# Kernel optimization log

Hardware: AMD Instinct MI355X
Metric: run time of the kernel (lower is better)

Reference implementation:

```python
import jax, jax.numpy as jnp
import numpy as np

N_USERS, N_ITEMS, D, B = 16384, 4096, 64, 2048
NAN_FRAC = 0.7
EPS = 1e-8


def setup_inputs() -> dict:
    key = jax.random.key(0)
    k1, k2, k3, k4, k5 = jax.random.split(key, 5)
    ratings = jax.random.uniform(k1, (N_USERS, N_ITEMS), jnp.float32, 1.0, 5.0)
    miss = jax.random.uniform(k2, (N_USERS, N_ITEMS)) < NAN_FRAC
    rating_matrix = jnp.where(miss, jnp.nan, ratings)
    user_embeddings = jax.random.normal(k3, (N_USERS, D), jnp.float32)
    user_indices = jax.random.randint(k4, (B,), 0, N_USERS)
    item_indices = jax.random.randint(k5, (B,), 0, N_ITEMS)
    return {
        "rating_matrix": rating_matrix,
        "user_embeddings": user_embeddings,
        "user_indices": user_indices,
        "item_indices": item_indices,
    }


def reference(rating_matrix, user_embeddings, user_indices, item_indices):
    n_users = rating_matrix.shape[0]

    # per-user average over non-NaN ratings (0.0 if user has no ratings)
    valid_r = ~jnp.isnan(rating_matrix)                      # [N, I]
    r0 = jnp.where(valid_r, rating_matrix, 0.0)
    cnt = valid_r.sum(axis=1)
    avg_ratings = jnp.where(cnt > 0, r0.sum(axis=1) / jnp.maximum(cnt, 1), 0.0)  # [N]

    u = user_embeddings[user_indices]                        # [B, d]
    # cosine similarity of each query user vs all users
    dots = jnp.einsum('bd,nd->bn', u, user_embeddings)       # [B, N]
    mag_u = jnp.linalg.norm(u, axis=1, keepdims=True)        # [B, 1]
    mag_v = jnp.linalg.norm(user_embeddings, axis=1)[None]   # [1, N]
    sim = dots / (mag_u * mag_v + EPS)                       # [B, N]

    # ratings of all users on each query item
    ratings_col = rating_matrix[:, item_indices].T           # [B, N]
    mask = ~jnp.isnan(ratings_col)                           # valid neighbor ratings
    mask = mask & (jnp.arange(n_users)[None, :] != user_indices[:, None])  # exclude self

    diff = jnp.where(mask, ratings_col - avg_ratings[None, :], 0.0)
    sim_m = jnp.where(mask, sim, 0.0)
    num = (diff * sim_m).sum(axis=1)                         # [B]
    den = jnp.abs(sim_m).sum(axis=1)                         # [B]
    den_safe = jnp.where(den == 0, 1.0, den)

    avg_u = avg_ratings[user_indices]
    return jnp.where(den == 0, avg_u, avg_u + num / den_safe)
```

## Files before the change

kernel.cpp:

```cpp
#include <hip/hip_runtime.h>
#include <math.h>

#define NU   16384
#define NI   4096
#define DDIM 64
#define BB   2048
#define GSTR8 2056

typedef unsigned short u16;
typedef unsigned char  u8;
typedef __attribute__((ext_vector_type(8))) short short8;
typedef __attribute__((ext_vector_type(4))) float f32x4;

static __device__ __forceinline__ u16 f2bf(float f) {
    union { float f; unsigned int u; } v; v.f = f;
    unsigned int u = v.u + 0x7FFFu + ((v.u >> 16) & 1u);
    return (u16)(u >> 16);
}

static __device__ __forceinline__ u8 enc_r(float r) {
    return (r == r) ? (u8)(__float2int_rn((r - 1.0f) * 50.0f) + 1) : (u8)0;
}

__global__ __launch_bounds__(256) void k_qprep(
    const float* __restrict__ E, const int* __restrict__ uidx,
    u16* __restrict__ Ubf, int2* __restrict__ qinfo)
{
    const int lane = threadIdx.x & 63;
    const int b = blockIdx.x * 4 + (threadIdx.x >> 6);
    const int ub = uidx[b];
    const float e = E[(size_t)ub * DDIM + lane];
    float ss = e * e;
#pragma unroll
    for (int o = 32; o > 0; o >>= 1) ss += __shfl_xor(ss, o);
    Ubf[b * DDIM + lane] = f2bf(e);
    if (lane == 0) qinfo[b] = make_int2(ub, __float_as_int(rsqrtf(ss)));
}

__global__ __launch_bounds__(256) void k_fused(
    const float* __restrict__ R, const float* __restrict__ E,
    const int* __restrict__ iidx, const u16* __restrict__ Ubf,
    const int2* __restrict__ qinfo, float2* __restrict__ partials,
    float* __restrict__ avgAll)
{
    __shared__ u16 s_ii[BB];
    __shared__ u8  rowq[2][NI];
    __shared__ u8  g[16][GSTR8];
    __shared__ float sAvg[16], sInv[16];
    __shared__ float redS[2][4], redC[2][4];

    const int tid  = threadIdx.x;
    const int lane = tid & 63;
    const int wid  = tid >> 6;
    const int n0   = blockIdx.x * 16;

    for (int t = tid; t < BB; t += 256) s_ii[t] = (u16)iidx[t];

#pragma unroll
    for (int rs = 0; rs < 4; ++rs) {
        const int n = n0 + wid * 4 + rs;
        const float e = E[(size_t)n * DDIM + lane];
        float ss = e * e;
#pragma unroll
        for (int o = 32; o > 0; o >>= 1) ss += __shfl_xor(ss, o);
        if (lane == 0) sInv[wid * 4 + rs] = rsqrtf(ss);
    }

    float4 vv[4];
    {
        const float4* R4 = (const float4*)(R + (size_t)n0 * NI);
#pragma unroll
        for (int j = 0; j < 4; ++j) vv[j] = R4[tid + j * 256];
    }

#pragma unroll 1
    for (int rr = 0; rr < 16; ++rr) {
        const int p = rr & 1;

        float4 vn[4];
        {
            const int np = n0 + ((rr < 15) ? rr + 1 : 15);
            const float4* Rn = (const float4*)(R + (size_t)np * NI);
#pragma unroll
            for (int j = 0; j < 4; ++j) vn[j] = Rn[tid + j * 256];
        }

        float sum = 0.f, cnt = 0.f;
#pragma unroll
        for (int j = 0; j < 4; ++j) {
            const float4 v = vv[j];
            if (v.x == v.x) { sum += v.x; cnt += 1.f; }
            if (v.y == v.y) { sum += v.y; cnt += 1.f; }
            if (v.z == v.z) { sum += v.z; cnt += 1.f; }
            if (v.w == v.w) { sum += v.w; cnt += 1.f; }
            uchar4 q;
            q.x = enc_r(v.x); q.y = enc_r(v.y); q.z = enc_r(v.z); q.w = enc_r(v.w);
            *(uchar4*)&rowq[p][(tid + j * 256) * 4] = q;
        }
#pragma unroll
        for (int o = 32; o > 0; o >>= 1) {
            sum += __shfl_xor(sum, o);
            cnt += __shfl_xor(cnt, o);
        }
        if (lane == 0) { redS[p][wid] = sum; redC[p][wid] = cnt; }

        __syncthreads();

        if (tid == 0) {
            const float S = redS[p][0] + redS[p][1] + redS[p][2] + redS[p][3];
            const float C = redC[p][0] + redC[p][1] + redC[p][2] + redC[p][3];
            const float a = (C > 0.f) ? (S / C) : 0.f;
            sAvg[rr] = a;
            avgAll[n0 + rr] = a;
        }
#pragma unroll
        for (int t = 0; t < 2; ++t) {
            const int b4 = (tid + t * 256) * 4;
            const ushort4 ii = *(const ushort4*)&s_ii[b4];
            uchar4 q;
            q.x = rowq[p][ii.x]; q.y = rowq[p][ii.y];
            q.z = rowq[p][ii.z]; q.w = rowq[p][ii.w];
            *(uchar4*)&g[rr][b4] = q;
        }
#pragma unroll
        for (int j = 0; j < 4; ++j) vv[j] = vn[j];
    }
    __syncthreads();

    const int lo = lane & 15;
    const int hi = lane >> 4;

    short8 a[2];
#pragma unroll
    for (int kg = 0; kg < 2; ++kg) {
        const float* ep = E + (size_t)(n0 + lo) * DDIM + kg * 32 + hi * 8;
        const float4 e0 = *(const float4*)(ep);
        const float4 e1 = *(const float4*)(ep + 4);
        union { short8 v; u16 u[8]; } t;
        t.u[0] = f2bf(e0.x); t.u[1] = f2bf(e0.y); t.u[2] = f2bf(e0.z); t.u[3] = f2bf(e0.w);
        t.u[4] = f2bf(e1.x); t.u[5] = f2bf(e1.y); t.u[6] = f2bf(e1.z); t.u[7] = f2bf(e1.w);
        a[kg] = t.v;
    }
    float avr[4], ivr[4];
#pragma unroll
    for (int r = 0; r < 4; ++r) { avr[r] = sAvg[hi * 4 + r]; ivr[r] = sInv[hi * 4 + r]; }

    float2* pout = partials + (size_t)blockIdx.x * BB;

#pragma unroll 1
    for (int j = 0; j < 32; ++j) {
        const int b0 = (j * 4 + wid) * 16;
        const int2 q = qinfo[b0 + lo];
        const float inv_mu = __int_as_float(q.y);

        const short8 bf0 = *(const short8*)(Ubf + (size_t)(b0 + lo) * DDIM + hi * 8);
        const short8 bf1 = *(const short8*)(Ubf + (size_t)(b0 + lo) * DDIM + 32 + hi * 8);

        f32x4 c = {0.f, 0.f, 0.f, 0.f};
        c = __builtin_amdgcn_mfma_f32_16x16x32_bf16(a[0], bf0, c, 0, 0, 0);
        c = __builtin_amdgcn_mfma_f32_16x16x32_bf16(a[1], bf1, c, 0, 0, 0);

        float fnum = 0.f, fden = 0.f;
#pragma unroll
        for (int r = 0; r < 4; ++r) {
            const int nr = n0 + hi * 4 + r;
            const u8 qg = g[hi * 4 + r][b0 + lo];
            const bool valid = (qg != 0) && (nr != q.x);
            const float gv = (float)(int)qg * 0.02f + 0.98f;
            const float s  = valid ? c[r] * (inv_mu * ivr[r]) : 0.f;
            fnum += (gv - avr[r]) * s;
            fden += fabsf(s);
        }
        fnum += __shfl_xor(fnum, 16); fden += __shfl_xor(fden, 16);
        fnum += __shfl_xor(fnum, 32); fden += __shfl_xor(fden, 32);
        if (lane < 16) pout[b0 + lane] = make_float2(fnum, fden);
    }
}

__global__ __launch_bounds__(256) void k_final(
    const float2* __restrict__ partials, const int2* __restrict__ qinfo,
    const float* __restrict__ avgAll, float* __restrict__ out)
{
    __shared__ float sn[8][32], sd[8][32];
    const int tid = threadIdx.x;
    const int bl  = tid & 31;
    const int ch  = tid >> 5;
    const int b   = blockIdx.x * 32 + bl;
    float n = 0.f, d = 0.f;
    for (int blk = ch; blk < NU / 16; blk += 8) {
        const float2 p = partials[(size_t)blk * BB + b];
        n += p.x; d += p.y;
    }
    sn[ch][bl] = n; sd[ch][bl] = d;
    __syncthreads();
    if (tid < 32) {
        float N = 0.f, D = 0.f;
#pragma unroll
        for (int c2 = 0; c2 < 8; ++c2) { N += sn[c2][tid]; D += sd[c2][tid]; }
        const int bb = blockIdx.x * 32 + tid;
        const float au = avgAll[qinfo[bb].x];
        out[bb] = (D == 0.f) ? au : (au + N / D);
    }
}

extern "C" void kernel_launch(void* const* d_in, const int* in_sizes, int n_in,
                              void* d_out, int out_size, void* d_ws, size_t ws_size,
                              hipStream_t stream)
{
    const float* R    = (const float*)d_in[0];
    const float* E    = (const float*)d_in[1];
    const int*   uidx = (const int*)d_in[2];
    const int*   iidx = (const int*)d_in[3];
    float* out = (float*)d_out;

    char* p = (char*)d_ws;
    float2* parts  = (float2*)p;  p += (size_t)(NU / 16) * BB * 8;
    u16*    Ubf    = (u16*)p;     p += (size_t)BB * DDIM * 2;
    int2*   qinfo  = (int2*)p;    p += (size_t)BB * 8;
    float*  avgAll = (float*)p;   p += (size_t)NU * 4;

    k_qprep<<<BB / 4, 256, 0, stream>>>(E, uidx, Ubf, qinfo);
    k_fused<<<NU / 16, 256, 0, stream>>>(R, E, iidx, Ubf, qinfo, parts, avgAll);
    k_final<<<BB / 32, 256, 0, stream>>>(parts, qinfo, avgAll, out);
}
```

Baseline: 455.1 us.

## Process rating rows per-wave without block barriers, using ballot counts and cheaper encoding

```diff
diff --git a/kernel.cpp b/kernel.cpp
--- a/kernel.cpp
+++ b/kernel.cpp
@@ -19,7 +19,7 @@
 }
 
 static __device__ __forceinline__ u8 enc_r(float r) {
-    return (r == r) ? (u8)(__float2int_rn((r - 1.0f) * 50.0f) + 1) : (u8)0;
+    return (u8)__float2uint_rz(fmaf(r, 50.f, -48.5f));
 }
 
 __global__ __launch_bounds__(256) void k_qprep(
@@ -44,10 +44,9 @@
     float* __restrict__ avgAll)
 {
     __shared__ u16 s_ii[BB];
-    __shared__ u8  rowq[2][NI];
+    __shared__ u8  wrow[4][NI];
     __shared__ u8  g[16][GSTR8];
     __shared__ float sAvg[16], sInv[16];
-    __shared__ float redS[2][4], redC[2][4];
 
     const int tid  = threadIdx.x;
     const int lane = tid & 63;
@@ -65,65 +64,56 @@
         for (int o = 32; o > 0; o >>= 1) ss += __shfl_xor(ss, o);
         if (lane == 0) sInv[wid * 4 + rs] = rsqrtf(ss);
     }
-
-    float4 vv[4];
-    {
-        const float4* R4 = (const float4*)(R + (size_t)n0 * NI);
-#pragma unroll
-        for (int j = 0; j < 4; ++j) vv[j] = R4[tid + j * 256];
-    }
+    __syncthreads();
 
 #pragma unroll 1
-    for (int rr = 0; rr < 16; ++rr) {
-        const int p = rr & 1;
-
-        float4 vn[4];
-        {
-            const int np = n0 + ((rr < 15) ? rr + 1 : 15);
-            const float4* Rn = (const float4*)(R + (size_t)np * NI);
-#pragma unroll
-            for (int j = 0; j < 4; ++j) vn[j] = Rn[tid + j * 256];
-        }
-
-        float sum = 0.f, cnt = 0.f;
-#pragma unroll
-        for (int j = 0; j < 4; ++j) {
-            const float4 v = vv[j];
-            if (v.x == v.x) { sum += v.x; cnt += 1.f; }
-            if (v.y == v.y) { sum += v.y; cnt += 1.f; }
-            if (v.z == v.z) { sum += v.z; cnt += 1.f; }
-            if (v.w == v.w) { sum += v.w; cnt += 1.f; }
+    for (int rs = 0; rs < 4; ++rs) {
+        const int rloc = wid * 4 + rs;
+        const int n = n0 + rloc;
+        const float4* R4 = (const float4*)(R + (size_t)n * NI);
+
+        float4 v[16];
+#pragma unroll
+        for (int j = 0; j < 16; ++j) v[j] = R4[j * 64 + lane];
+
+        float sum = 0.f;
+        unsigned cnti = 0;
+#pragma unroll
+        for (int j = 0; j < 16; ++j) {
+            const float4 x = v[j];
+            sum += (x.x == x.x ? x.x : 0.f);
+            sum += (x.y == x.y ? x.y : 0.f);
+            sum += (x.z == x.z ? x.z : 0.f);
+            sum += (x.w == x.w ? x.w : 0.f);
+            cnti += (unsigned)__popcll(__ballot(x.x == x.x));
+            cnti += (unsigned)__popcll(__ballot(x.y == x.y));
+            cnti += (unsigned)__popcll(__ballot(x.z == x.z));
+            cnti += (unsigned)__popcll(__ballot(x.w == x.w));
             uchar4 q;
-            q.x = enc_r(v.x); q.y = enc_r(v.y); q.z = enc_r(v.z); q.w = enc_r(v.w);
-            *(uchar4*)&rowq[p][(tid + j * 256) * 4] = q;
-        }
-#pragma unroll
-        for (int o = 32; o > 0; o >>= 1) {
-            sum += __shfl_xor(sum, o);
-            cnt += __shfl_xor(cnt, o);
-        }
-        if (lane == 0) { redS[p][wid] = sum; redC[p][wid] = cnt; }
-
-        __syncthreads();
-
-        if (tid == 0) {
-            const float S = redS[p][0] + redS[p][1] + redS[p][2] + redS[p][3];
-            const float C = redC[p][0] + redC[p][1] + redC[p][2] + redC[p][3];
-            const float a = (C > 0.f) ? (S / C) : 0.f;
-            sAvg[rr] = a;
-            avgAll[n0 + rr] = a;
-        }
-#pragma unroll
-        for (int t = 0; t < 2; ++t) {
-            const int b4 = (tid + t * 256) * 4;
+            q.x = enc_r(x.x); q.y = enc_r(x.y); q.z = enc_r(x.z); q.w = enc_r(x.w);
+            *(uchar4*)&wrow[wid][(j * 64 + lane) * 4] = q;
+        }
+#pragma unroll
+        for (int o = 32; o > 0; o >>= 1) sum += __shfl_xor(sum, o);
+        if (lane == 0) {
+            const float C = (float)cnti;
+            const float a = (C > 0.f) ? (sum / C) : 0.f;
+            sAvg[rloc] = a;
+            avgAll[n] = a;
+        }
+        asm volatile("s_waitcnt lgkmcnt(0)" ::: "memory");
+
+#pragma unroll
+        for (int t = 0; t < 8; ++t) {
+            const int b4 = (t * 64 + lane) * 4;
             const ushort4 ii = *(const ushort4*)&s_ii[b4];
             uchar4 q;
-            q.x = rowq[p][ii.x]; q.y = rowq[p][ii.y];
-            q.z = rowq[p][ii.z]; q.w = rowq[p][ii.w];
-            *(uchar4*)&g[rr][b4] = q;
-        }
-#pragma unroll
-        for (int j = 0; j < 4; ++j) vv[j] = vn[j];
+            q.x = wrow[wid][ii.x];
+            q.y = wrow[wid][ii.y];
+            q.z = wrow[wid][ii.z];
+            q.w = wrow[wid][ii.w];
+            *(uchar4*)&g[rloc][b4] = q;
+        }
     }
     __syncthreads();
 
```

Measured after the change: 457.3 us. No clear change (+0.5%).
